# Kernel optimization log

Hardware: AMD Instinct MI355X
Metric: run time of the kernel (lower is better)

The kernel has to match this reference:

```python
import jax, jax.numpy as jnp
import numpy as np

D_MODEL = 1024
NUM_HEADS = 16
D_K = D_MODEL // NUM_HEADS


def setup_inputs() -> dict:
    key = jax.random.key(0)
    ks = jax.random.split(key, 5)
    s = 1.0 / np.sqrt(D_MODEL)
    return {
        "x": jax.random.normal(ks[0], (1, 4096, D_MODEL), dtype=jnp.float32),
        "w_qkv": jax.random.uniform(ks[1], (D_MODEL, 3 * D_MODEL), jnp.float32, -s, s),
        "b_qkv": jax.random.uniform(ks[2], (3 * D_MODEL,), jnp.float32, -s, s),
        "w_out": jax.random.uniform(ks[3], (D_MODEL, D_MODEL), jnp.float32, -s, s),
        "b_out": jax.random.uniform(ks[4], (D_MODEL,), jnp.float32, -s, s),
    }


def reference(x, w_qkv, b_qkv, w_out, b_out):
    B, S, D = x.shape
    H, dk = NUM_HEADS, D_K
    qkv = x @ w_qkv + b_qkv                      # [B,S,3D]
    qkv = qkv.reshape(B, S, 3, H, dk)
    qkv = jnp.transpose(qkv, (2, 0, 3, 1, 4))     # [3,B,H,S,dk]
    q, k, v = qkv[0], qkv[1], qkv[2]
    scores = jnp.einsum('bhqd,bhkd->bhqk', q, k) / jnp.sqrt(jnp.float32(dk))
    attn = jax.nn.softmax(scores, axis=-1)        # [B,H,S,S] -- 1 GB, memory-bound
    out = jnp.einsum('bhqk,bhkd->bhqd', attn, v)  # [B,H,S,dk]
    out = jnp.transpose(out, (0, 2, 1, 3)).reshape(B, S, D)
    return out @ w_out + b_out
```

## Files before the change

### kernel.cpp

```cpp
#include <hip/hip_runtime.h>
#include <stdint.h>
#include <stddef.h>

typedef __bf16 bf16;
typedef uint32_t u32;
typedef __attribute__((ext_vector_type(8))) __bf16 bf16x8;
typedef __attribute__((ext_vector_type(4))) __bf16 bf16x4;
typedef __attribute__((ext_vector_type(4))) float f32x4;
typedef __attribute__((ext_vector_type(16))) float f32x16;
typedef __attribute__((ext_vector_type(8))) unsigned short u16x8;
typedef __attribute__((ext_vector_type(4))) u32 u32x4;

__device__ __forceinline__ void gload_lds16(const void* g, void* l) {
  __builtin_amdgcn_global_load_lds(
      (const __attribute__((address_space(1))) unsigned int*)g,
      (__attribute__((address_space(3))) unsigned int*)l, 16, 0, 0);
}

__device__ __forceinline__ float fast_exp2(float x) {
#if __has_builtin(__builtin_amdgcn_exp2f)
  return __builtin_amdgcn_exp2f(x);
#else
  float r; asm("v_exp_f32 %0, %1" : "=v"(r) : "v"(x)); return r;
#endif
}

__device__ __forceinline__ u32 cvtpk_bf16(float lo, float hi_) {
  u32 r;
  asm("v_cvt_pk_bf16_f32 %0, %1, %2" : "=v"(r) : "v"(lo), "v"(hi_));
  return r;
}

__device__ __forceinline__ void pl32swap(u32& a, u32& b) {
  asm("v_permlane32_swap_b32 %0, %1" : "+v"(a), "+&v"(b));
}

__device__ __forceinline__ float xhalf_max(float v) {
  return fmaxf(v, __shfl_xor(v, 32, 64));
}
__device__ __forceinline__ float xhalf_sum(float v) {
  return v + __shfl_xor(v, 32, 64);
}

__global__ void cvt_bf16_kernel(const float* __restrict__ in, bf16* __restrict__ out, int n) {
  int i = (blockIdx.x * blockDim.x + threadIdx.x) * 4;
  if (i < n) {
    float4 v = *(const float4*)(in + i);
    bf16x4 o;
    o[0] = (bf16)v.x; o[1] = (bf16)v.y; o[2] = (bf16)v.z; o[3] = (bf16)v.w;
    *(bf16x4*)(out + i) = o;
  }
}

__global__ void transpose_cvt_kernel(const float* __restrict__ in, bf16* __restrict__ out,
                                     int K_, int N_) {
  __shared__ __align__(16) bf16 t[64][65];
  const int nb = blockIdx.x * 64, kb = blockIdx.y * 64;
  const int c = threadIdx.x & 63, r0 = (threadIdx.x >> 6) * 16;
#pragma unroll
  for (int i = 0; i < 16; ++i) {
    int rr = r0 + i;
    t[c][rr] = (bf16)in[(size_t)(kb + rr) * N_ + nb + c];
  }
  __syncthreads();
#pragma unroll
  for (int i = 0; i < 16; ++i) {
    int rr = r0 + i;
    out[(size_t)(nb + rr) * K_ + kb + c] = t[rr][c];
  }
}

#define BM 128
#define BN 128
#define BK 64

template <int MODE>
__global__ __launch_bounds__(256) void gemm_bt(
    const bf16* __restrict__ A, const bf16* __restrict__ BT,
    const float* __restrict__ bias, void* __restrict__ Cout,
    int M, int N, int K, float qscale, int qcols) {
  __shared__ __align__(16) bf16 As[BM * BK];
  __shared__ __align__(16) bf16 Bs[BN * BK];
  const int tid = threadIdx.x;
  const int lane = tid & 63;
  const int w = tid >> 6;
  const int wm = (w >> 1) * 64;
  const int wn = (w & 1) * 64;
  const int m0 = blockIdx.x * BM;
  const int n0 = blockIdx.y * BN;
  const int r = lane & 15, g = lane >> 4;

  f32x4 acc[4][4] = {};

  for (int k0 = 0; k0 < K; k0 += BK) {
    __syncthreads();
#pragma unroll
    for (int i = 0; i < 4; ++i) {
      int id = tid + i * 256;
      int row = id >> 3, c = id & 7;
      int sc = c ^ (row & 7);
      gload_lds16(A + (size_t)(m0 + row) * K + k0 + sc * 8, As + id * 8);
      gload_lds16(BT + (size_t)(n0 + row) * K + k0 + sc * 8, Bs + id * 8);
    }
    __syncthreads();
#pragma unroll
    for (int s = 0; s < 2; ++s) {
      bf16x8 fa[4], fb[4];
#pragma unroll
      for (int i = 0; i < 4; ++i) {
        int arow = wm + i * 16 + r;
        fa[i] = *(const bf16x8*)(As + arow * 64 + (((s * 4 + g) ^ (arow & 7)) << 3));
        int brow = wn + i * 16 + r;
        fb[i] = *(const bf16x8*)(Bs + brow * 64 + (((s * 4 + g) ^ (brow & 7)) << 3));
      }
#pragma unroll
      for (int i = 0; i < 4; ++i)
#pragma unroll
        for (int j = 0; j < 4; ++j)
          acc[i][j] = __builtin_amdgcn_mfma_f32_16x16x32_bf16(fa[i], fb[j], acc[i][j], 0, 0, 0);
    }
  }

#pragma unroll
  for (int i = 0; i < 4; ++i) {
#pragma unroll
    for (int j = 0; j < 4; ++j) {
      int col = n0 + wn + j * 16 + r;
      float b = bias[col];
      float sc = (MODE == 0 && col < qcols) ? qscale : 1.0f;
#pragma unroll
      for (int rr = 0; rr < 4; ++rr) {
        int row = m0 + wm + i * 16 + g * 4 + rr;
        float v = (acc[i][j][rr] + b) * sc;
        if (MODE == 0)
          ((bf16*)Cout)[(size_t)row * N + col] = (bf16)v;
        else
          ((float*)Cout)[(size_t)row * N + col] = v;
      }
    }
  }
}

#define LDQ 3072

__global__ __launch_bounds__(512, 4) void attn_fwd4(const bf16* __restrict__ qkv,
                                                    bf16* __restrict__ out) {
  __shared__ __align__(16) bf16 Kl[2][2][64 * 64];
  __shared__ __align__(16) bf16 Vt[2][2][64 * 64];
  __shared__ float ml[4][32][2];

  const int tid = threadIdx.x, lane = tid & 63, w = tid >> 6;
  const int hi = lane >> 5, q = lane & 31;
  const int qt = w & 3, half = w >> 2;
  const int h = blockIdx.y;
  const int q0 = blockIdx.x * 128 + qt * 32;

  const bf16* Qg = qkv + h * 64;
  const bf16* Kg = qkv + 1024 + h * 64;
  const bf16* Vg = qkv + 2048 + h * 64;

  bf16x8 fq[4];
  {
    const bf16* qp = Qg + (size_t)(q0 + q) * LDQ + hi * 8;
#pragma unroll
    for (int st = 0; st < 4; ++st) fq[st] = *(const bf16x8*)(qp + st * 16);
  }

  const int krow = tid >> 3, kc = tid & 7;
  const int ksc = kc ^ (krow & 7);
  const int vhalf = tid >> 8;
  const int t2 = tid & 255;
  const int kvp = t2 & 31, dgh = t2 >> 5;
  const int kv0 = kvp * 2;

  bf16x8 vreg0, vreg1;

  auto issue_k = [&](int it, int buf) {
#pragma unroll
    for (int i = 0; i < 2; ++i)
      gload_lds16(Kg + (size_t)(i * 2048 + it * 64 + krow) * LDQ + ksc * 8,
                  &Kl[buf][i][tid * 8]);
  };
  auto load_v = [&](int it) {
    const bf16* vp = Vg + (size_t)(vhalf * 2048 + it * 64 + kv0) * LDQ + dgh * 8;
    vreg0 = *(const bf16x8*)vp;
    vreg1 = *(const bf16x8*)(vp + LDQ);
  };
  auto stage_v = [&](int buf) {
    bf16* base = &Vt[buf][vhalf][0];
    u16x8 lo = __builtin_bit_cast(u16x8, vreg0);
    u16x8 hb = __builtin_bit_cast(u16x8, vreg1);
#pragma unroll
    for (int jj = 0; jj < 8; ++jj) {
      int d = dgh * 8 + jj;
      u32 pk = (u32)lo[jj] | ((u32)hb[jj] << 16);
      *(u32*)(base + d * 64 + (((kvp >> 2) ^ (d & 7)) << 3) + (kv0 & 7)) = pk;
    }
  };

  issue_k(0, 0);
  load_v(0);
  stage_v(0);

  f32x16 o0 = {}, o1 = {};
  float m_run = -1e30f, l_run = 0.f;
  __syncthreads();

  for (int it = 0; it < 32; ++it) {
    const int cur = it & 1, nxt = cur ^ 1;
    const bool pf = (it < 31);

    if (pf) { issue_k(it + 1, nxt); load_v(it + 1); }

    const bf16* kb = &Kl[cur][half][0];
    f32x16 p0 = {}, p1 = {};
    __builtin_amdgcn_s_setprio(1);
#pragma unroll
    for (int st = 0; st < 4; ++st) {
      bf16x8 ka0 = *(const bf16x8*)(kb + q * 64 + (((2 * st + hi) ^ (q & 7)) << 3));
      bf16x8 ka1 = *(const bf16x8*)(kb + (32 + q) * 64 + (((2 * st + hi) ^ (q & 7)) << 3));
      p0 = __builtin_amdgcn_mfma_f32_32x32x16_bf16(ka0, fq[st], p0, 0, 0, 0);
      p1 = __builtin_amdgcn_mfma_f32_32x32x16_bf16(ka1, fq[st], p1, 0, 0, 0);
    }
    __builtin_amdgcn_s_setprio(0);

    float t16[16];
#pragma unroll
    for (int i = 0; i < 16; ++i) t16[i] = fmaxf(p0[i], p1[i]);
#pragma unroll
    for (int s2 = 8; s2 > 0; s2 >>= 1)
#pragma unroll
      for (int i = 0; i < s2; ++i) t16[i] = fmaxf(t16[i], t16[i + s2]);
    float mx = xhalf_max(t16[0]);

    if (__any(mx > m_run + 8.0f)) {
      float mnew = fmaxf(m_run, mx);
      float alpha = fast_exp2(m_run - mnew);
      l_run *= alpha;
#pragma unroll
      for (int i = 0; i < 16; ++i) { o0[i] *= alpha; o1[i] *= alpha; }
      m_run = mnew;
    }

#pragma unroll
    for (int i = 0; i < 16; ++i) p0[i] = fast_exp2(p0[i] - m_run);
#pragma unroll
    for (int i = 0; i < 16; ++i) p1[i] = fast_exp2(p1[i] - m_run);

    float s8[8];
#pragma unroll
    for (int i = 0; i < 8; ++i) s8[i] = (p0[i] + p0[i + 8]) + (p1[i] + p1[i + 8]);
#pragma unroll
    for (int s2 = 4; s2 > 0; s2 >>= 1)
#pragma unroll
      for (int i = 0; i < s2; ++i) s8[i] += s8[i + s2];
    l_run += xhalf_sum(s8[0]);

    u32x4 pb[4];
#pragma unroll
    for (int hf = 0; hf < 2; ++hf) {
#pragma unroll
      for (int qd = 0; qd < 2; ++qd) {
        int ks = hf * 2 + qd;
        u32 a0, b0, a1, b1;
        if (hf == 0) {
          a0 = cvtpk_bf16(p0[qd * 8 + 0], p0[qd * 8 + 1]);
          b0 = cvtpk_bf16(p0[qd * 8 + 4], p0[qd * 8 + 5]);
          a1 = cvtpk_bf16(p0[qd * 8 + 2], p0[qd * 8 + 3]);
          b1 = cvtpk_bf16(p0[qd * 8 + 6], p0[qd * 8 + 7]);
        } else {
          a0 = cvtpk_bf16(p1[qd * 8 + 0], p1[qd * 8 + 1]);
          b0 = cvtpk_bf16(p1[qd * 8 + 4], p1[qd * 8 + 5]);
          a1 = cvtpk_bf16(p1[qd * 8 + 2], p1[qd * 8 + 3]);
          b1 = cvtpk_bf16(p1[qd * 8 + 6], p1[qd * 8 + 7]);
        }
        pl32swap(a0, b0);
        pl32swap(a1, b1);
        pb[ks][0] = a0; pb[ks][1] = a1; pb[ks][2] = b0; pb[ks][3] = b1;
      }
    }

    const bf16* vb = &Vt[cur][half][0];
    __builtin_amdgcn_s_setprio(1);
#pragma unroll
    for (int ks = 0; ks < 4; ++ks) {
      bf16x8 pf2 = __builtin_bit_cast(bf16x8, pb[ks]);
      int ck = ((2 * ks + hi) ^ (q & 7)) << 3;
      bf16x8 av0 = *(const bf16x8*)(vb + q * 64 + ck);
      bf16x8 av1 = *(const bf16x8*)(vb + (32 + q) * 64 + ck);
      o0 = __builtin_amdgcn_mfma_f32_32x32x16_bf16(av0, pf2, o0, 0, 0, 0);
      o1 = __builtin_amdgcn_mfma_f32_32x32x16_bf16(av1, pf2, o1, 0, 0, 0);
    }
    __builtin_amdgcn_s_setprio(0);

    if (pf) stage_v(nxt);
    __syncthreads();
  }

  float* comb = (float*)&Kl[0][0][0];
  if (half == 1) {
    float* dst = comb + qt * 2048 + lane * 32;
#pragma unroll
    for (int c = 0; c < 8; ++c) {
      f32x4 v;
      if (c < 4) { v[0] = o0[c*4+0]; v[1] = o0[c*4+1]; v[2] = o0[c*4+2]; v[3] = o0[c*4+3]; }
      else       { v[0] = o1[(c-4)*4+0]; v[1] = o1[(c-4)*4+1]; v[2] = o1[(c-4)*4+2]; v[3] = o1[(c-4)*4+3]; }
      *(f32x4*)(dst + c * 4) = v;
    }
    if (hi == 0) { ml[qt][q][0] = m_run; ml[qt][q][1] = l_run; }
  }
  __syncthreads();
  if (half == 0) {
    const float* src = comb + qt * 2048 + lane * 32;
    float mB = ml[qt][q][0], lB = ml[qt][q][1];
    float m = fmaxf(m_run, mB);
    float wA = fast_exp2(m_run - m), wB = fast_exp2(mB - m);
    float linv = 1.0f / (l_run * wA + lB * wB);
    wA *= linv; wB *= linv;
    bf16* op = out + (size_t)(q0 + q) * 1024 + h * 64;
#pragma unroll
    for (int c = 0; c < 8; ++c) {
      f32x4 ob = *(const f32x4*)(src + c * 4);
      float e0, e1, e2, e3;
      if (c < 4) { e0 = o0[c*4+0]; e1 = o0[c*4+1]; e2 = o0[c*4+2]; e3 = o0[c*4+3]; }
      else       { e0 = o1[(c-4)*4+0]; e1 = o1[(c-4)*4+1]; e2 = o1[(c-4)*4+2]; e3 = o1[(c-4)*4+3]; }
      e0 = e0 * wA + ob[0] * wB;
      e1 = e1 * wA + ob[1] * wB;
      e2 = e2 * wA + ob[2] * wB;
      e3 = e3 * wA + ob[3] * wB;
      int db = c >> 2, rg = c & 3;
      int dbase = db * 32 + rg * 8 + hi * 4;
      uint2 stv;
      stv.x = cvtpk_bf16(e0, e1);
      stv.y = cvtpk_bf16(e2, e3);
      *(uint2*)(op + dbase) = stv;
    }
  }
}

extern "C" void kernel_launch(void* const* d_in, const int* in_sizes, int n_in,
                              void* d_out, int out_size, void* d_ws, size_t ws_size,
                              hipStream_t stream) {
  const float* x     = (const float*)d_in[0];
  const float* w_qkv = (const float*)d_in[1];
  const float* b_qkv = (const float*)d_in[2];
  const float* w_out = (const float*)d_in[3];
  const float* b_out = (const float*)d_in[4];
  float* outp = (float*)d_out;

  char* ws = (char*)d_ws;
  bf16* qkv   = (bf16*)(ws);
  bf16* xbf   = (bf16*)(ws + 24u * 1024 * 1024);
  bf16* wqkvT = (bf16*)(ws + 32u * 1024 * 1024);
  bf16* woutT = (bf16*)(ws + 38u * 1024 * 1024);

  cvt_bf16_kernel<<<4096, 256, 0, stream>>>(x, xbf, 4096 * 1024);
  transpose_cvt_kernel<<<dim3(48, 16), 256, 0, stream>>>(w_qkv, wqkvT, 1024, 3072);
  transpose_cvt_kernel<<<dim3(16, 16), 256, 0, stream>>>(w_out, woutT, 1024, 1024);

  gemm_bt<0><<<dim3(32, 24), 256, 0, stream>>>(xbf, wqkvT, b_qkv, qkv,
                                               4096, 3072, 1024,
                                               0.125f * 1.44269504088896f, 1024);

  attn_fwd4<<<dim3(32, 16), 512, 0, stream>>>(qkv, xbf);

  gemm_bt<1><<<dim3(32, 8), 256, 0, stream>>>(xbf, woutT, b_out, outp,
                                              4096, 1024, 1024, 1.0f, 0);
}
```

Before: 182.6 us.

## Split attention softmax into two sub-tiles, pad V layout, swizzle block order

The attention inner loop now handles the two 32-key score halves one after the other: max, exp, convert, then PV MFMA for the first half before the second half's softmax. This lets the first PV MFMAs overlap the second half's VALU work. The transposed V tile uses a padded row stride of 68 instead of an XOR swizzle, read as two 8-byte loads, and the grid is flattened with a block-index swizzle that spreads heads across XCDs. The split adds a second rescale check and more 8-byte LDS reads, and the padding may introduce bank conflicts.

```diff
diff --git a/kernel.cpp b/kernel.cpp
--- a/kernel.cpp
+++ b/kernel.cpp
@@ -40,6 +40,10 @@
 }
 __device__ __forceinline__ float xhalf_sum(float v) {
   return v + __shfl_xor(v, 32, 64);
+}
+
+__device__ __forceinline__ float max3f(float a, float b, float c) {
+  return fmaxf(fmaxf(a, b), c);
 }
 
 __global__ void cvt_bf16_kernel(const float* __restrict__ in, bf16* __restrict__ out, int n) {
@@ -142,18 +146,22 @@
 }
 
 #define LDQ 3072
-
-__global__ __launch_bounds__(512, 4) void attn_fwd4(const bf16* __restrict__ qkv,
+#define VSTR 68
+
+__global__ __launch_bounds__(512, 4) void attn_fwd5(const bf16* __restrict__ qkv,
                                                     bf16* __restrict__ out) {
   __shared__ __align__(16) bf16 Kl[2][2][64 * 64];
-  __shared__ __align__(16) bf16 Vt[2][2][64 * 64];
+  __shared__ __align__(16) bf16 Vt[2][2][64 * VSTR];
   __shared__ float ml[4][32][2];
 
   const int tid = threadIdx.x, lane = tid & 63, w = tid >> 6;
   const int hi = lane >> 5, q = lane & 31;
   const int qt = w & 3, half = w >> 2;
-  const int h = blockIdx.y;
-  const int q0 = blockIdx.x * 128 + qt * 32;
+
+  const int bid = blockIdx.x;
+  const int swz = (bid & 7) * 64 + (bid >> 3);
+  const int h = swz >> 5, qb = swz & 31;
+  const int q0 = qb * 128 + qt * 32;
 
   const bf16* Qg = qkv + h * 64;
   const bf16* Kg = qkv + 1024 + h * 64;
@@ -194,8 +202,14 @@
     for (int jj = 0; jj < 8; ++jj) {
       int d = dgh * 8 + jj;
       u32 pk = (u32)lo[jj] | ((u32)hb[jj] << 16);
-      *(u32*)(base + d * 64 + (((kvp >> 2) ^ (d & 7)) << 3) + (kv0 & 7)) = pk;
-    }
+      *(u32*)(base + d * VSTR + kv0) = pk;
+    }
+  };
+  auto ldV = [&](const bf16* vb, int row, int ks) -> bf16x8 {
+    const bf16* p = vb + row * VSTR + ks * 16 + hi * 8;
+    bf16x4 lo = *(const bf16x4*)p;
+    bf16x4 hb = *(const bf16x4*)(p + 4);
+    return __builtin_shufflevector(lo, hb, 0, 1, 2, 3, 4, 5, 6, 7);
   };
 
   issue_k(0, 0);
@@ -208,92 +222,125 @@
 
   for (int it = 0; it < 32; ++it) {
     const int cur = it & 1, nxt = cur ^ 1;
-    const bool pf = (it < 31);
-
-    if (pf) { issue_k(it + 1, nxt); load_v(it + 1); }
+    const bool pfch = (it < 31);
+
+    if (pfch) { issue_k(it + 1, nxt); load_v(it + 1); }
 
     const bf16* kb = &Kl[cur][half][0];
+    const bf16* vb = &Vt[cur][half][0];
+
     f32x16 p0 = {}, p1 = {};
     __builtin_amdgcn_s_setprio(1);
 #pragma unroll
     for (int st = 0; st < 4; ++st) {
       bf16x8 ka0 = *(const bf16x8*)(kb + q * 64 + (((2 * st + hi) ^ (q & 7)) << 3));
+      p0 = __builtin_amdgcn_mfma_f32_32x32x16_bf16(ka0, fq[st], p0, 0, 0, 0);
+    }
+#pragma unroll
+    for (int st = 0; st < 4; ++st) {
       bf16x8 ka1 = *(const bf16x8*)(kb + (32 + q) * 64 + (((2 * st + hi) ^ (q & 7)) << 3));
-      p0 = __builtin_amdgcn_mfma_f32_32x32x16_bf16(ka0, fq[st], p0, 0, 0, 0);
       p1 = __builtin_amdgcn_mfma_f32_32x32x16_bf16(ka1, fq[st], p1, 0, 0, 0);
     }
     __builtin_amdgcn_s_setprio(0);
 
-    float t16[16];
-#pragma unroll
-    for (int i = 0; i < 16; ++i) t16[i] = fmaxf(p0[i], p1[i]);
-#pragma unroll
-    for (int s2 = 8; s2 > 0; s2 >>= 1)
-#pragma unroll
-      for (int i = 0; i < s2; ++i) t16[i] = fmaxf(t16[i], t16[i + s2]);
-    float mx = xhalf_max(t16[0]);
-
-    if (__any(mx > m_run + 8.0f)) {
-      float mnew = fmaxf(m_run, mx);
+    float a0 = max3f(p0[0], p0[1], p0[2]);
+    float a1 = max3f(p0[3], p0[4], p0[5]);
+    float a2 = max3f(p0[6], p0[7], p0[8]);
+    float a3 = max3f(p0[9], p0[10], p0[11]);
+    float a4 = max3f(p0[12], p0[13], p0[14]);
+    float mxa = xhalf_max(max3f(max3f(a0, a1, a2), max3f(a3, a4, p0[15]), -1e30f));
+
+    if (__any(mxa > m_run + 8.0f)) {
+      float mnew = fmaxf(m_run, mxa);
       float alpha = fast_exp2(m_run - mnew);
       l_run *= alpha;
 #pragma unroll
       for (int i = 0; i < 16; ++i) { o0[i] *= alpha; o1[i] *= alpha; }
       m_run = mnew;
     }
-
 #pragma unroll
     for (int i = 0; i < 16; ++i) p0[i] = fast_exp2(p0[i] - m_run);
+
+    float sa[8];
+#pragma unroll
+    for (int i = 0; i < 8; ++i) sa[i] = p0[i] + p0[i + 8];
+#pragma unroll
+    for (int s2 = 4; s2 > 0; s2 >>= 1)
+#pragma unroll
+      for (int i = 0; i < s2; ++i) sa[i] += sa[i + s2];
+    float psum = sa[0];
+
+    u32x4 pb[4];
+#pragma unroll
+    for (int qd = 0; qd < 2; ++qd) {
+      u32 c0 = cvtpk_bf16(p0[qd * 8 + 0], p0[qd * 8 + 1]);
+      u32 d0 = cvtpk_bf16(p0[qd * 8 + 4], p0[qd * 8 + 5]);
+      u32 c1 = cvtpk_bf16(p0[qd * 8 + 2], p0[qd * 8 + 3]);
+      u32 d1 = cvtpk_bf16(p0[qd * 8 + 6], p0[qd * 8 + 7]);
+      pl32swap(c0, d0);
+      pl32swap(c1, d1);
+      pb[qd][0] = c0; pb[qd][1] = c1; pb[qd][2] = d0; pb[qd][3] = d1;
+    }
+
+    __builtin_amdgcn_s_setprio(1);
+#pragma unroll
+    for (int ks = 0; ks < 2; ++ks) {
+      bf16x8 pf2 = __builtin_bit_cast(bf16x8, pb[ks]);
+      o0 = __builtin_amdgcn_mfma_f32_32x32x16_bf16(ldV(vb, q, ks), pf2, o0, 0, 0, 0);
+      o1 = __builtin_amdgcn_mfma_f32_32x32x16_bf16(ldV(vb, 32 + q, ks), pf2, o1, 0, 0, 0);
+    }
+    __builtin_amdgcn_s_setprio(0);
+
+    float b0 = max3f(p1[0], p1[1], p1[2]);
+    float b1 = max3f(p1[3], p1[4], p1[5]);
+    float b2 = max3f(p1[6], p1[7], p1[8]);
+    float b3 = max3f(p1[9], p1[10], p1[11]);
+    float b4 = max3f(p1[12], p1[13], p1[14]);
+    float mxb = xhalf_max(max3f(max3f(b0, b1, b2), max3f(b3, b4, p1[15]), -1e30f));
+
+    if (__any(mxb > m_run + 8.0f)) {
+      float mnew = fmaxf(m_run, mxb);
+      float alpha = fast_exp2(m_run - mnew);
+      l_run *= alpha;
+      psum *= alpha;
+#pragma unroll
+      for (int i = 0; i < 16; ++i) { o0[i] *= alpha; o1[i] *= alpha; }
+      m_run = mnew;
+    }
 #pragma unroll
     for (int i = 0; i < 16; ++i) p1[i] = fast_exp2(p1[i] - m_run);
 
-    float s8[8];
-#pragma unroll
-    for (int i = 0; i < 8; ++i) s8[i] = (p0[i] + p0[i + 8]) + (p1[i] + p1[i + 8]);
+    float sb[8];
+#pragma unroll
+    for (int i = 0; i < 8; ++i) sb[i] = p1[i] + p1[i + 8];
 #pragma unroll
     for (int s2 = 4; s2 > 0; s2 >>= 1)
 #pragma unroll
-      for (int i = 0; i < s2; ++i) s8[i] += s8[i + s2];
-    l_run += xhalf_sum(s8[0]);
-
-    u32x4 pb[4];
-#pragma unroll
-    for (int hf = 0; hf < 2; ++hf) {
-#pragma unroll
-      for (int qd = 0; qd < 2; ++qd) {
-        int ks = hf * 2 + qd;
-        u32 a0, b0, a1, b1;
-        if (hf == 0) {
-          a0 = cvtpk_bf16(p0[qd * 8 + 0], p0[qd * 8 + 1]);
-          b0 = cvtpk_bf16(p0[qd * 8 + 4], p0[qd * 8 + 5]);
-          a1 = cvtpk_bf16(p0[qd * 8 + 2], p0[qd * 8 + 3]);
-          b1 = cvtpk_bf16(p0[qd * 8 + 6], p0[qd * 8 + 7]);
-        } else {
-          a0 = cvtpk_bf16(p1[qd * 8 + 0], p1[qd * 8 + 1]);
-          b0 = cvtpk_bf16(p1[qd * 8 + 4], p1[qd * 8 + 5]);
-          a1 = cvtpk_bf16(p1[qd * 8 + 2], p1[qd * 8 + 3]);
-          b1 = cvtpk_bf16(p1[qd * 8 + 6], p1[qd * 8 + 7]);
-        }
-        pl32swap(a0, b0);
-        pl32swap(a1, b1);
-        pb[ks][0] = a0; pb[ks][1] = a1; pb[ks][2] = b0; pb[ks][3] = b1;
-      }
-    }
-
-    const bf16* vb = &Vt[cur][half][0];
+      for (int i = 0; i < s2; ++i) sb[i] += sb[i + s2];
+
+    l_run += xhalf_sum(psum + sb[0]);
+
+#pragma unroll
+    for (int qd = 0; qd < 2; ++qd) {
+      u32 c0 = cvtpk_bf16(p1[qd * 8 + 0], p1[qd * 8 + 1]);
+      u32 d0 = cvtpk_bf16(p1[qd * 8 + 4], p1[qd * 8 + 5]);
+      u32 c1 = cvtpk_bf16(p1[qd * 8 + 2], p1[qd * 8 + 3]);
+      u32 d1 = cvtpk_bf16(p1[qd * 8 + 6], p1[qd * 8 + 7]);
+      pl32swap(c0, d0);
+      pl32swap(c1, d1);
+      pb[2 + qd][0] = c0; pb[2 + qd][1] = c1; pb[2 + qd][2] = d0; pb[2 + qd][3] = d1;
+    }
+
     __builtin_amdgcn_s_setprio(1);
 #pragma unroll
-    for (int ks = 0; ks < 4; ++ks) {
+    for (int ks = 2; ks < 4; ++ks) {
       bf16x8 pf2 = __builtin_bit_cast(bf16x8, pb[ks]);
-      int ck = ((2 * ks + hi) ^ (q & 7)) << 3;
-      bf16x8 av0 = *(const bf16x8*)(vb + q * 64 + ck);
-      bf16x8 av1 = *(const bf16x8*)(vb + (32 + q) * 64 + ck);
-      o0 = __builtin_amdgcn_mfma_f32_32x32x16_bf16(av0, pf2, o0, 0, 0, 0);
-      o1 = __builtin_amdgcn_mfma_f32_32x32x16_bf16(av1, pf2, o1, 0, 0, 0);
+      o0 = __builtin_amdgcn_mfma_f32_32x32x16_bf16(ldV(vb, q, ks), pf2, o0, 0, 0, 0);
+      o1 = __builtin_amdgcn_mfma_f32_32x32x16_bf16(ldV(vb, 32 + q, ks), pf2, o1, 0, 0, 0);
     }
     __builtin_amdgcn_s_setprio(0);
 
-    if (pf) stage_v(nxt);
+    if (pfch) stage_v(nxt);
     __syncthreads();
   }
 
@@ -362,7 +409,7 @@
                                                4096, 3072, 1024,
                                                0.125f * 1.44269504088896f, 1024);
 
-  attn_fwd4<<<dim3(32, 16), 512, 0, stream>>>(qkv, xbf);
+  attn_fwd5<<<512, 512, 0, stream>>>(qkv, xbf);
 
   gemm_bt<1><<<dim3(32, 8), 256, 0, stream>>>(xbf, woutT, b_out, outp,
                                               4096, 1024, 1024, 1.0f, 0);
```

Result: faster. 176.1 us (-3.6%).
